# Optimization experiments

Hardware: AMD Instinct MI355X
Metric: run time of the kernel (lower is better)

The kernel has to match this reference:

```python
import jax, jax.numpy as jnp
import numpy as np

B, N = 32, 25200          # batch, anchors (YOLOX @ 1280, strides 8/16/32)
NUM_CLASSES = 80
CH = 5 + NUM_CLASSES
CONF_THRE = 0.7
NMS_THRE = 0.45
TOPK = 512                # fixed pre-/post-NMS candidate budget (jit-static)
CLASS_OFFSET = 4096.0     # class-offset trick from the torch code


def setup_inputs() -> dict:
    key = jax.random.key(0)
    pred = jax.random.uniform(key, (B, N, CH), dtype=jnp.float32)
    # put box coords in pixel scale so IoU/NMS behaves realistically
    pred = pred.at[..., :4].multiply(640.0)
    return {"prediction": pred}


def _pairwise_iou(boxes):
    # boxes: [K, 4] xyxy -> iou: [K, K] (same math as torchvision.ops.nms)
    x1, y1, x2, y2 = boxes[:, 0], boxes[:, 1], boxes[:, 2], boxes[:, 3]
    area = (x2 - x1) * (y2 - y1)
    iw = jnp.clip(jnp.minimum(x2[:, None], x2[None, :]) - jnp.maximum(x1[:, None], x1[None, :]), 0.0)
    ih = jnp.clip(jnp.minimum(y2[:, None], y2[None, :]) - jnp.maximum(y1[:, None], y1[None, :]), 0.0)
    inter = iw * ih
    return inter / (area[:, None] + area[None, :] - inter)


def _greedy_nms(boxes, valid, iou_thre):
    # boxes are pre-sorted by descending score; greedy suppression identical to torchvision NMS
    iou = _pairwise_iou(boxes)  # [K, K]
    idx = jnp.arange(boxes.shape[0])

    def body(i, keep):
        suppress = (iou[i] > iou_thre) & (idx > i) & keep[i]
        return keep & ~suppress

    return jax.lax.fori_loop(0, boxes.shape[0], body, valid)


def _per_image(pred):
    # pred: [N, 5+C]
    cx, cy, w, h = pred[:, 0], pred[:, 1], pred[:, 2], pred[:, 3]
    hw, hh = w * 0.5, h * 0.5
    boxes = jnp.stack([cx - hw, cy - hh, cx + hw, cy + hh], axis=1)  # [N, 4] xyxy

    cls_scores = pred[:, 5:5 + NUM_CLASSES]
    class_conf = jnp.max(cls_scores, axis=1)
    class_pred = jnp.argmax(cls_scores, axis=1)
    conf = pred[:, 4] * class_conf                      # obj * class score
    valid = conf >= CONF_THRE

    # confidence filter + sort-by-score via fixed-size top-k (invalids ranked last)
    rank = jnp.where(valid, conf, -1.0)
    _, order = jax.lax.top_k(rank, TOPK)                # [TOPK], descending score
    b = boxes[order]
    c = conf[order]
    cl = class_pred[order]
    v = valid[order]

    nms_boxes = b + cl.astype(b.dtype)[:, None] * CLASS_OFFSET
    keep = _greedy_nms(nms_boxes, v, NMS_THRE)          # [TOPK] bool

    det = jnp.concatenate([b, c[:, None], cl.astype(jnp.float32)[:, None]], axis=1)  # [TOPK, 6]
    det = det * jax.lax.stop_gradient(keep.astype(det.dtype))[:, None]
    return det, keep


def reference(prediction):
    # returns padded detections [B, TOPK, 6] (x1,y1,x2,y2,conf,cls) and keep mask [B, TOPK]
    det, keep = jax.vmap(_per_image)(prediction)
    return det, keep
```

## Files before the change

kernel.cpp:

```cpp
#include <hip/hip_runtime.h>
#include <stdint.h>

#define BATCH 32
#define NANCH 25200
#define CH 85
#define NCLS 80
#define TOPK 512
#define CONF_THRE 0.7f
#define NMS_THRE 0.45f
#define CLS_OFF 4096.0f

typedef unsigned long long u64;
typedef unsigned int u32;

#define OFF_CONF  0
#define OFF_NMS   3225600
#define OFF_DET   3553280
#define OFF_VALID 3946496
#define OFF_MASK  3948544

__global__ __launch_bounds__(256) void scan_kernel(const float* __restrict__ pred,
                                                   u32* __restrict__ conf32) {
    const int tid = threadIdx.x;
    const int lane = tid & 63;
    const int wv = tid >> 6;
    const int g = lane >> 4;
    const int l = lane & 15;
    const int a = blockIdx.x * 16 + wv * 4 + g;
    const size_t base = (size_t)a * CH;

    float m = -1.0f, obj = 0.0f;
    {
        const float4 q = *(const float4*)(pred + base + (l << 2));
        const int p = l << 2;
        if (p + 0 >= 5) m = fmaxf(m, q.x); else if (p + 0 == 4) obj = q.x;
        if (p + 1 >= 5) m = fmaxf(m, q.y); else if (p + 1 == 4) obj = q.y;
        if (p + 2 >= 5) m = fmaxf(m, q.z); else if (p + 2 == 4) obj = q.z;
        if (p + 3 >= 5) m = fmaxf(m, q.w); else if (p + 3 == 4) obj = q.w;
    }
    if (l < 5) {
        const float4 q = *(const float4*)(pred + base + 64 + (l << 2));
        m = fmaxf(fmaxf(m, fmaxf(q.x, q.y)), fmaxf(q.z, q.w));
    } else if (l == 5) {
        m = fmaxf(m, pred[base + 84]);
    }
    #pragma unroll
    for (int off = 1; off < 16; off <<= 1) m = fmaxf(m, __shfl_xor(m, off));
    const float ob = __shfl(obj, (lane & 48) + 1);
    const float conf = ob * m;
    if (l == 0)
        conf32[a] = (conf >= CONF_THRE) ? __float_as_uint(conf) : 0u;
}

__global__ __launch_bounds__(1024) void select_kernel(const float* __restrict__ pred,
                                                      const u32* __restrict__ conf32,
                                                      float* __restrict__ nmsG,
                                                      float* __restrict__ detG,
                                                      u64* __restrict__ validG) {
    __shared__ u64 sbuf[1024];
    __shared__ u64 sorted[1024];
    __shared__ u32 hist[256];
    __shared__ u32 wtot[4];
    __shared__ u32 s_cnt, s_pivot;
    __shared__ unsigned char val[TOPK];

    const int img = blockIdx.x;
    const int tid = threadIdx.x;
    const int lane = tid & 63;
    const int wv = tid >> 6;

    if (tid == 0) { s_cnt = 0u; s_pivot = 0u; }
    if (tid < 256) hist[tid] = 0u;
    __syncthreads();

    const uint4* cd4 = (const uint4*)(conf32 + (size_t)img * NANCH);

    for (int i = tid; i < NANCH / 4; i += 1024) {
        const uint4 q = cd4[i];
        if (q.x) atomicAdd(&hist[(q.x >> 15) & 255u], 1u);
        if (q.y) atomicAdd(&hist[(q.y >> 15) & 255u], 1u);
        if (q.z) atomicAdd(&hist[(q.z >> 15) & 255u], 1u);
        if (q.w) atomicAdd(&hist[(q.w >> 15) & 255u], 1u);
    }
    __syncthreads();

    u32 v = 0, s = 0;
    if (tid < 256) {
        v = hist[tid]; s = v;
        #pragma unroll
        for (int off = 1; off < 64; off <<= 1) {
            const u32 t = __shfl_down(s, off);
            if (lane + off < 64) s += t;
        }
        if (lane == 0) wtot[wv] = s;
    }
    __syncthreads();
    if (tid < 256) {
        u32 add = 0;
        for (int w2 = wv + 1; w2 < 4; ++w2) add += wtot[w2];
        const u32 sfull = s + add;
        const u32 snext = sfull - v;
        if (sfull >= TOPK && snext < TOPK) s_pivot = (u32)tid;
    }
    __syncthreads();
    const u32 T = 0x3F000000u | (s_pivot << 15);

    for (int i = tid; i < NANCH / 4; i += 1024) {
        const uint4 q = cd4[i];
        const u32 a0 = (u32)(i << 2);
        if (q.x >= T) { const u32 p = atomicAdd(&s_cnt, 1u);
            if (p < 1024u) sbuf[p] = ((u64)q.x << 32) | (u64)(0xFFFFFFFFu - a0); }
        if (q.y >= T) { const u32 p = atomicAdd(&s_cnt, 1u);
            if (p < 1024u) sbuf[p] = ((u64)q.y << 32) | (u64)(0xFFFFFFFFu - (a0 + 1)); }
        if (q.z >= T) { const u32 p = atomicAdd(&s_cnt, 1u);
            if (p < 1024u) sbuf[p] = ((u64)q.z << 32) | (u64)(0xFFFFFFFFu - (a0 + 2)); }
        if (q.w >= T) { const u32 p = atomicAdd(&s_cnt, 1u);
            if (p < 1024u) sbuf[p] = ((u64)q.w << 32) | (u64)(0xFFFFFFFFu - (a0 + 3)); }
    }
    __syncthreads();
    const u32 mc = (s_cnt > 1024u) ? 1024u : s_cnt;

    sorted[tid] = 0ull;
    u32 rank = 0; u64 my = 0ull;
    if (tid < (int)mc) {
        my = sbuf[tid];
        for (u32 i = 0; i < mc; ++i) rank += (sbuf[i] > my) ? 1u : 0u;
    }
    __syncthreads();
    if (tid < (int)mc && rank < 1024u) sorted[rank] = my;
    __syncthreads();

    const int g = lane >> 3;
    const int l = lane & 7;
    float* nb_ = nmsG + (size_t)img * (5 * TOPK);
    float* dt_ = detG + (size_t)img * (6 * TOPK);
    for (int pass = 0; pass < 4; ++pass) {
        const int r = pass * 128 + wv * 8 + g;
        const u64 key = sorted[r];
        const float conf = __uint_as_float((u32)(key >> 32));
        const bool okrow = conf >= CONF_THRE;
        float x1 = 0.f, y1 = 0.f, x2 = 0.f, y2 = 0.f, clsf = 0.f;
        if (okrow) {
            const u32 anchor = 0xFFFFFFFFu - (u32)(key & 0xFFFFFFFFull);
            const float* row = pred + ((size_t)img * NANCH + anchor) * CH;
            float vs[10];
            #pragma unroll
            for (int k = 0; k < 10; ++k) vs[k] = row[5 + l + 8 * k];
            float4 box;
            if (l == 0) box = *(const float4*)row;
            float vv = vs[0];
            int ci = l;
            #pragma unroll
            for (int k = 1; k < 10; ++k)
                if (vs[k] > vv) { vv = vs[k]; ci = 8 * k + l; }
            #pragma unroll
            for (int off = 4; off > 0; off >>= 1) {
                const float ov = __shfl_xor(vv, off);
                const int oi = __shfl_xor(ci, off);
                if (ov > vv || (ov == vv && oi < ci)) { vv = ov; ci = oi; }
            }
            if (l == 0) {
                const float hw = box.z * 0.5f, hh = box.w * 0.5f;
                x1 = box.x - hw; y1 = box.y - hh; x2 = box.x + hw; y2 = box.y + hh;
                clsf = (float)ci;
            }
        }
        if (l == 0) {
            const float off = clsf * CLS_OFF;
            const float X1 = x1 + off, Y1 = y1 + off, X2 = x2 + off, Y2 = y2 + off;
            nb_[0 * TOPK + r] = X1; nb_[1 * TOPK + r] = Y1;
            nb_[2 * TOPK + r] = X2; nb_[3 * TOPK + r] = Y2;
            nb_[4 * TOPK + r] = (X2 - X1) * (Y2 - Y1);
            dt_[r * 6 + 0] = x1; dt_[r * 6 + 1] = y1;
            dt_[r * 6 + 2] = x2; dt_[r * 6 + 3] = y2;
            dt_[r * 6 + 4] = okrow ? conf : 0.0f;
            dt_[r * 6 + 5] = clsf;
            val[r] = okrow ? 1 : 0;
        }
    }
    __syncthreads();

    if (tid < TOPK) {
        const u64 vb = __ballot(val[tid] != 0);
        if (lane == 0) validG[img * 8 + wv] = vb;
    }
}

__global__ __launch_bounds__(256) void iou_kernel(const float* __restrict__ nmsG,
                                                  u64* __restrict__ maskG) {
    __shared__ float bx1[TOPK], by1[TOPK], bx2[TOPK], by2[TOPK], bar[TOPK];
    const int img = blockIdx.x;
    const int slab = blockIdx.y;
    const int tid = threadIdx.x;
    const int lane = tid & 63;
    const float* nb_ = nmsG + (size_t)img * (5 * TOPK);
    for (int i = tid; i < TOPK; i += 256) {
        bx1[i] = nb_[i];            by1[i] = nb_[TOPK + i];
        bx2[i] = nb_[2 * TOPK + i]; by2[i] = nb_[3 * TOPK + i];
        bar[i] = nb_[4 * TOPK + i];
    }
    __syncthreads();
    const int q0 = slab * (16 * TOPK);
    for (int q = q0 + tid; q < q0 + 16 * TOPK; q += 256) {
        const int i = q >> 9;
        const int j = q & (TOPK - 1);
        bool sup = false;
        if (j > i) {
            const float xx1 = fmaxf(bx1[i], bx1[j]);
            const float yy1 = fmaxf(by1[i], by1[j]);
            const float xx2 = fminf(bx2[i], bx2[j]);
            const float yy2 = fminf(by2[i], by2[j]);
            const float iw = fmaxf(xx2 - xx1, 0.0f);
            const float ih = fmaxf(yy2 - yy1, 0.0f);
            const float inter = iw * ih;
            const float uni = bar[i] + bar[j] - inter;
            const float iou = inter / uni;
            sup = iou > NMS_THRE;
        }
        const u64 bm = __ballot(sup);
        if (lane == 0) maskG[(size_t)img * 4096 + (q >> 6)] = bm;
    }
}

__global__ __launch_bounds__(256) void greedy_kernel(const u64* __restrict__ maskG,
                                                     const u64* __restrict__ validG,
                                                     const float* __restrict__ detG,
                                                     float* __restrict__ out) {
    __shared__ u64 m[TOPK * 8];
    __shared__ u64 kw8[8];
    const int img = blockIdx.x;
    const int tid = threadIdx.x;
    const int lane = tid & 63;
    const int wv = tid >> 6;
    const u64* mg = maskG + (size_t)img * 4096;
    for (int i = tid; i < 4096; i += 256) m[i] = mg[i];
    __syncthreads();

    if (wv == 0) {
        const bool ld = lane < 8;
        u64 kw = ld ? validG[img * 8 + lane] : 0ull;
        u64 p0 = ld ? m[0 * 8 + lane] : 0ull;
        u64 p1 = ld ? m[1 * 8 + lane] : 0ull;
        u64 p2 = ld ? m[2 * 8 + lane] : 0ull;
        u64 p3 = ld ? m[3 * 8 + lane] : 0ull;
        for (int i = 0; i < TOPK; i += 4) {
            {
                const u64 w = __shfl(kw, i >> 6);
                const u64 bit = (w >> (i & 63)) & 1ull;
                kw &= ~(p0 & (0ull - bit));
                p0 = (ld && i + 4 < TOPK) ? m[(i + 4) * 8 + lane] : 0ull;
            }
            {
                const u64 w = __shfl(kw, (i + 1) >> 6);
                const u64 bit = (w >> ((i + 1) & 63)) & 1ull;
                kw &= ~(p1 & (0ull - bit));
                p1 = (ld && i + 5 < TOPK) ? m[(i + 5) * 8 + lane] : 0ull;
            }
            {
                const u64 w = __shfl(kw, (i + 2) >> 6);
                const u64 bit = (w >> ((i + 2) & 63)) & 1ull;
                kw &= ~(p2 & (0ull - bit));
                p2 = (ld && i + 6 < TOPK) ? m[(i + 6) * 8 + lane] : 0ull;
            }
            {
                const u64 w = __shfl(kw, (i + 3) >> 6);
                const u64 bit = (w >> ((i + 3) & 63)) & 1ull;
                kw &= ~(p3 & (0ull - bit));
                p3 = (ld && i + 7 < TOPK) ? m[(i + 7) * 8 + lane] : 0ull;
            }
        }
        if (ld) kw8[lane] = kw;
    }
    __syncthreads();

    const float* dt_ = detG + (size_t)img * (6 * TOPK);
    float* det_out = out + (size_t)img * (TOPK * 6);
    float* keep_out = out + (size_t)BATCH * TOPK * 6 + (size_t)img * TOPK;
    for (int idx = tid; idx < TOPK * 6; idx += 256) {
        const int r = idx / 6;
        const float kf = ((kw8[r >> 6] >> (r & 63)) & 1ull) ? 1.0f : 0.0f;
        det_out[idx] = dt_[idx] * kf;
    }
    for (int r = tid; r < TOPK; r += 256) {
        keep_out[r] = ((kw8[r >> 6] >> (r & 63)) & 1ull) ? 1.0f : 0.0f;
    }
}

extern "C" void kernel_launch(void* const* d_in, const int* in_sizes, int n_in,
                              void* d_out, int out_size, void* d_ws, size_t ws_size,
                              hipStream_t stream) {
    const float* pred = (const float*)d_in[0];
    float* out = (float*)d_out;
    char* ws = (char*)d_ws;
    u32* conf32 = (u32*)(ws + OFF_CONF);
    float* nmsG = (float*)(ws + OFF_NMS);
    float* detG = (float*)(ws + OFF_DET);
    u64* validG = (u64*)(ws + OFF_VALID);
    u64* maskG = (u64*)(ws + OFF_MASK);

    scan_kernel<<<(BATCH * NANCH) / 16, 256, 0, stream>>>(pred, conf32);
    select_kernel<<<BATCH, 1024, 0, stream>>>(pred, conf32, nmsG, detG, validG);
    dim3 g4(BATCH, 32);
    iou_kernel<<<g4, 256, 0, stream>>>(nmsG, maskG);
    greedy_kernel<<<BATCH, 256, 0, stream>>>(maskG, validG, detG, out);
}
```

Measured before the change: 439.1 us.

## Fuse IoU mask and greedy NMS kernels into one per-image block

Merges the separate IoU-mask kernel and the greedy-suppression kernel into a single 1024-thread kernel per image. The suppression bitmask now stays in shared memory instead of going through a global round trip, and one kernel launch is removed. Each wave also keeps its j-box coordinates in registers and loops over 32 rows. The cost is lower parallelism: only 32 blocks now compute the IoU matrix, where before 32x32 blocks did.

```diff
diff --git a/kernel.cpp b/kernel.cpp
--- a/kernel.cpp
+++ b/kernel.cpp
@@ -17,7 +17,6 @@
 #define OFF_NMS   3225600
 #define OFF_DET   3553280
 #define OFF_VALID 3946496
-#define OFF_MASK  3948544
 
 __global__ __launch_bounds__(256) void scan_kernel(const float* __restrict__ pred,
                                                    u32* __restrict__ conf32) {
@@ -186,87 +185,89 @@
     }
 }
 
-__global__ __launch_bounds__(256) void iou_kernel(const float* __restrict__ nmsG,
-                                                  u64* __restrict__ maskG) {
+__global__ __launch_bounds__(1024) void nms_kernel(const float* __restrict__ nmsG,
+                                                   const u64* __restrict__ validG,
+                                                   const float* __restrict__ detG,
+                                                   float* __restrict__ out) {
     __shared__ float bx1[TOPK], by1[TOPK], bx2[TOPK], by2[TOPK], bar[TOPK];
-    const int img = blockIdx.x;
-    const int slab = blockIdx.y;
-    const int tid = threadIdx.x;
-    const int lane = tid & 63;
-    const float* nb_ = nmsG + (size_t)img * (5 * TOPK);
-    for (int i = tid; i < TOPK; i += 256) {
-        bx1[i] = nb_[i];            by1[i] = nb_[TOPK + i];
-        bx2[i] = nb_[2 * TOPK + i]; by2[i] = nb_[3 * TOPK + i];
-        bar[i] = nb_[4 * TOPK + i];
-    }
-    __syncthreads();
-    const int q0 = slab * (16 * TOPK);
-    for (int q = q0 + tid; q < q0 + 16 * TOPK; q += 256) {
-        const int i = q >> 9;
-        const int j = q & (TOPK - 1);
-        bool sup = false;
-        if (j > i) {
-            const float xx1 = fmaxf(bx1[i], bx1[j]);
-            const float yy1 = fmaxf(by1[i], by1[j]);
-            const float xx2 = fminf(bx2[i], bx2[j]);
-            const float yy2 = fminf(by2[i], by2[j]);
-            const float iw = fmaxf(xx2 - xx1, 0.0f);
-            const float ih = fmaxf(yy2 - yy1, 0.0f);
-            const float inter = iw * ih;
-            const float uni = bar[i] + bar[j] - inter;
-            const float iou = inter / uni;
-            sup = iou > NMS_THRE;
-        }
-        const u64 bm = __ballot(sup);
-        if (lane == 0) maskG[(size_t)img * 4096 + (q >> 6)] = bm;
-    }
-}
-
-__global__ __launch_bounds__(256) void greedy_kernel(const u64* __restrict__ maskG,
-                                                     const u64* __restrict__ validG,
-                                                     const float* __restrict__ detG,
-                                                     float* __restrict__ out) {
-    __shared__ u64 m[TOPK * 8];
+    __shared__ u64 smask[TOPK * 8];
     __shared__ u64 kw8[8];
     const int img = blockIdx.x;
     const int tid = threadIdx.x;
     const int lane = tid & 63;
     const int wv = tid >> 6;
-    const u64* mg = maskG + (size_t)img * 4096;
-    for (int i = tid; i < 4096; i += 256) m[i] = mg[i];
+
+    const float* nb_ = nmsG + (size_t)img * (5 * TOPK);
+    if (tid < TOPK) {
+        bx1[tid] = nb_[tid];            by1[tid] = nb_[TOPK + tid];
+        bx2[tid] = nb_[2 * TOPK + tid]; by2[tid] = nb_[3 * TOPK + tid];
+        bar[tid] = nb_[4 * TOPK + tid];
+    }
+    __syncthreads();
+
+    float jx1[8], jy1[8], jx2[8], jy2[8], jar[8];
+    #pragma unroll
+    for (int jb = 0; jb < 8; ++jb) {
+        const int j = jb * 64 + lane;
+        jx1[jb] = bx1[j]; jy1[jb] = by1[j];
+        jx2[jb] = bx2[j]; jy2[jb] = by2[j];
+        jar[jb] = bar[j];
+    }
+    for (int i = wv * 32; i < wv * 32 + 32; ++i) {
+        const float ix1 = bx1[i], iy1 = by1[i], ix2 = bx2[i], iy2 = by2[i], iar = bar[i];
+        #pragma unroll
+        for (int jb = 0; jb < 8; ++jb) {
+            const int j = jb * 64 + lane;
+            bool sup = false;
+            if (j > i) {
+                const float xx1 = fmaxf(ix1, jx1[jb]);
+                const float yy1 = fmaxf(iy1, jy1[jb]);
+                const float xx2 = fminf(ix2, jx2[jb]);
+                const float yy2 = fminf(iy2, jy2[jb]);
+                const float iw = fmaxf(xx2 - xx1, 0.0f);
+                const float ih = fmaxf(yy2 - yy1, 0.0f);
+                const float inter = iw * ih;
+                const float uni = iar + jar[jb] - inter;
+                const float iou = inter / uni;
+                sup = iou > NMS_THRE;
+            }
+            const u64 bm = __ballot(sup);
+            if (lane == 0) smask[i * 8 + jb] = bm;
+        }
+    }
     __syncthreads();
 
     if (wv == 0) {
         const bool ld = lane < 8;
         u64 kw = ld ? validG[img * 8 + lane] : 0ull;
-        u64 p0 = ld ? m[0 * 8 + lane] : 0ull;
-        u64 p1 = ld ? m[1 * 8 + lane] : 0ull;
-        u64 p2 = ld ? m[2 * 8 + lane] : 0ull;
-        u64 p3 = ld ? m[3 * 8 + lane] : 0ull;
+        u64 p0 = ld ? smask[0 * 8 + lane] : 0ull;
+        u64 p1 = ld ? smask[1 * 8 + lane] : 0ull;
+        u64 p2 = ld ? smask[2 * 8 + lane] : 0ull;
+        u64 p3 = ld ? smask[3 * 8 + lane] : 0ull;
         for (int i = 0; i < TOPK; i += 4) {
             {
                 const u64 w = __shfl(kw, i >> 6);
                 const u64 bit = (w >> (i & 63)) & 1ull;
                 kw &= ~(p0 & (0ull - bit));
-                p0 = (ld && i + 4 < TOPK) ? m[(i + 4) * 8 + lane] : 0ull;
+                p0 = (ld && i + 4 < TOPK) ? smask[(i + 4) * 8 + lane] : 0ull;
             }
             {
                 const u64 w = __shfl(kw, (i + 1) >> 6);
                 const u64 bit = (w >> ((i + 1) & 63)) & 1ull;
                 kw &= ~(p1 & (0ull - bit));
-                p1 = (ld && i + 5 < TOPK) ? m[(i + 5) * 8 + lane] : 0ull;
+                p1 = (ld && i + 5 < TOPK) ? smask[(i + 5) * 8 + lane] : 0ull;
             }
             {
                 const u64 w = __shfl(kw, (i + 2) >> 6);
                 const u64 bit = (w >> ((i + 2) & 63)) & 1ull;
                 kw &= ~(p2 & (0ull - bit));
-                p2 = (ld && i + 6 < TOPK) ? m[(i + 6) * 8 + lane] : 0ull;
+                p2 = (ld && i + 6 < TOPK) ? smask[(i + 6) * 8 + lane] : 0ull;
             }
             {
                 const u64 w = __shfl(kw, (i + 3) >> 6);
                 const u64 bit = (w >> ((i + 3) & 63)) & 1ull;
                 kw &= ~(p3 & (0ull - bit));
-                p3 = (ld && i + 7 < TOPK) ? m[(i + 7) * 8 + lane] : 0ull;
+                p3 = (ld && i + 7 < TOPK) ? smask[(i + 7) * 8 + lane] : 0ull;
             }
         }
         if (ld) kw8[lane] = kw;
@@ -276,13 +277,13 @@
     const float* dt_ = detG + (size_t)img * (6 * TOPK);
     float* det_out = out + (size_t)img * (TOPK * 6);
     float* keep_out = out + (size_t)BATCH * TOPK * 6 + (size_t)img * TOPK;
-    for (int idx = tid; idx < TOPK * 6; idx += 256) {
+    for (int idx = tid; idx < TOPK * 6; idx += 1024) {
         const int r = idx / 6;
         const float kf = ((kw8[r >> 6] >> (r & 63)) & 1ull) ? 1.0f : 0.0f;
         det_out[idx] = dt_[idx] * kf;
     }
-    for (int r = tid; r < TOPK; r += 256) {
-        keep_out[r] = ((kw8[r >> 6] >> (r & 63)) & 1ull) ? 1.0f : 0.0f;
+    if (tid < TOPK) {
+        keep_out[tid] = ((kw8[tid >> 6] >> (tid & 63)) & 1ull) ? 1.0f : 0.0f;
     }
 }
 
@@ -296,11 +297,8 @@
     float* nmsG = (float*)(ws + OFF_NMS);
     float* detG = (float*)(ws + OFF_DET);
     u64* validG = (u64*)(ws + OFF_VALID);
-    u64* maskG = (u64*)(ws + OFF_MASK);
 
     scan_kernel<<<(BATCH * NANCH) / 16, 256, 0, stream>>>(pred, conf32);
     select_kernel<<<BATCH, 1024, 0, stream>>>(pred, conf32, nmsG, detG, validG);
-    dim3 g4(BATCH, 32);
-    iou_kernel<<<g4, 256, 0, stream>>>(nmsG, maskG);
-    greedy_kernel<<<BATCH, 256, 0, stream>>>(maskG, validG, detG, out);
+    nms_kernel<<<BATCH, 1024, 0, stream>>>(nmsG, validG, detG, out);
 }
```

Result: slower. 451.8 us (+2.9%).
